# Kernel tuning notes

Measured on AMD Instinct MI355X. Metric: run time of the kernel, lower is better.

## Reference

```python
import jax, jax.numpy as jnp
import numpy as np

EPS = 1e-8


def setup_inputs() -> dict:
    key = jax.random.key(0)
    k1, k2 = jax.random.split(key)
    B, C, L = 16, 4, 4096
    K, S = 256, 128
    x = jax.random.normal(k1, (B, C, L), dtype=jnp.float32)
    shapelets = jax.random.normal(k2, (C, K, S), dtype=jnp.float32)
    return {"x": x, "shapelets": shapelets}


def reference(x, shapelets):
    # x: (B, C, L); shapelets: (C, K, S)
    B, C, L = x.shape
    _, K, S = shapelets.shape
    W = L - S + 1  # number of sliding windows

    # unfold: (B, C, W, S) sliding windows with stride 1
    idx = jnp.arange(W)[:, None] + jnp.arange(S)[None, :]  # (W, S)
    win = x[:, :, idx]  # (B, C, W, S)
    win = win / jnp.maximum(jnp.linalg.norm(win, axis=-1, keepdims=True), EPS)

    shp = shapelets / jnp.maximum(
        jnp.linalg.norm(shapelets, axis=-1, keepdims=True), EPS
    )  # (C, K, S)

    # pairwise dot products: (B, C, W, K)
    sim = jnp.einsum("bcws,cks->bcwk", win, shp)
    # sum over channels, keepdim, transpose(2,3), divide by n_dims
    sim = jnp.sum(sim, axis=1, keepdims=True) / C  # (B, 1, W, K)
    sim = jnp.transpose(sim, (0, 1, 3, 2))  # (B, 1, K, W)
    sim = jax.nn.relu(sim)
    # global max-pool over window positions -> (B, 1, K)
    return jnp.max(sim, axis=3)
```

## Files before the change

kernel.cpp:

```cpp
#include <hip/hip_runtime.h>
#include <hip/hip_bf16.h>

#define NB 16
#define NC 4
#define NL 4096
#define NK 256
#define NS 128
#define NW (NL - NS + 1)
#define WPB 512
#define KPB 128
#define XEL 640
#define XROW 656
#define EPSF 1e-8f

typedef __attribute__((ext_vector_type(8))) _Float16 f16x8;
typedef __attribute__((ext_vector_type(2))) _Float16 f16x2;
typedef __attribute__((ext_vector_type(4))) float floatx4;

typedef __attribute__((address_space(3))) unsigned int* lds_ptr_t;
typedef const __attribute__((address_space(1))) unsigned int* gbl_ptr_t;

__device__ inline short f2h(float f) {
    _Float16 h = (_Float16)f;
    short s;
    __builtin_memcpy(&s, &h, sizeof(short));
    return s;
}

__device__ inline void gload_lds16(const void* g, void* l) {
    __builtin_amdgcn_global_load_lds((gbl_ptr_t)g, (lds_ptr_t)l, 16, 0, 0);
}

__global__ __launch_bounds__(64)
void norm_shp_kernel(const float* __restrict__ shp, short* __restrict__ shpn) {
    int ck = blockIdx.x;
    int k = ck & (NK - 1);
    int lane = threadIdx.x;
    const float* p = shp + (size_t)ck * NS;
    float v0 = p[lane];
    float v1 = p[lane + 64];
    float ss = v0 * v0 + v1 * v1;
    #pragma unroll
    for (int o = 32; o > 0; o >>= 1) ss += __shfl_xor(ss, o, 64);
    float rn = 1.f / fmaxf(sqrtf(ss), EPSF);
    int s0 = lane, s1 = lane + 64;
    int d0 = ((((s0 >> 3) ^ (k & 15)) << 3) | (s0 & 7));
    int d1 = ((((s1 >> 3) ^ (k & 15)) << 3) | (s1 & 7));
    shpn[(size_t)ck * NS + d0] = f2h(v0 * rn);
    shpn[(size_t)ck * NS + d1] = f2h(v1 * rn);
}

__global__ __launch_bounds__(512, 1)
void mcs_main_kernel(const float* __restrict__ x,
                     const short* __restrict__ shpn,
                     float* __restrict__ out) {
    __shared__ f16x8 bs[NC][KPB * 16];
    __shared__ alignas(16) short xcp[NC][4][XROW];
    __shared__ union {
        float scratch[NC][XEL];
        struct { float invw[NC][WPB]; float epi[8][64]; } c;
    } u;

    const int kq = blockIdx.x, slot = blockIdx.y;
    const int b = slot >> 3, wslot = slot & 7;
    const int w0 = wslot * WPB;
    const int tid = threadIdx.x;
    const int lane = tid & 63, wv = tid >> 6;
    const int m = lane & 15, q = lane >> 4, r = m & 3;
    const int kh = wv & 1, wh = wv >> 1;

    {
        const char* gbase = (const char*)shpn + (size_t)(kq * KPB) * NS * 2;
        #pragma unroll
        for (int c = 0; c < NC; c++) {
            const char* gc = gbase + (size_t)c * NK * NS * 2;
            char* lc = (char*)&bs[c][0];
            #pragma unroll
            for (int i = 0; i < 4; i++) {
                int off = (wv * 4 + i) * 1024;
                gload_lds16(gc + off + lane * 16, lc + off);
            }
        }
    }

    float xv[NC], xv2[NC];
    {
        const int g0 = w0 + tid;
        #pragma unroll
        for (int c = 0; c < NC; c++)
            xv[c] = (g0 < NL) ? x[((size_t)b * NC + c) * NL + g0] : 0.f;
        if (tid < XEL - 512) {
            const int g1 = g0 + 512;
            #pragma unroll
            for (int c = 0; c < NC; c++)
                xv2[c] = (g1 < NL) ? x[((size_t)b * NC + c) * NL + g1] : 0.f;
        }
    }

    #pragma unroll
    for (int c = 0; c < NC; c++) {
        short hv = f2h(xv[c]);
        #pragma unroll
        for (int rr = 0; rr < 4; rr++) {
            int o2 = tid - rr;
            if (o2 >= 0) xcp[c][rr][o2] = hv;
        }
        u.scratch[c][tid] = xv[c] * xv[c];
        if (tid < XEL - 512) {
            short hv2 = f2h(xv2[c]);
            #pragma unroll
            for (int rr = 0; rr < 4; rr++)
                xcp[c][rr][tid + 512 - rr] = hv2;
            u.scratch[c][tid + 512] = xv2[c] * xv2[c];
        }
    }
    __syncthreads();

    if (wv < 4) {
        const int c = wv;
        const int base = lane * 10;
        float v[10];
        #pragma unroll
        for (int i = 0; i < 10; i++) v[i] = u.scratch[c][base + i];
        #pragma unroll
        for (int i = 1; i < 10; i++) v[i] += v[i - 1];
        float tt = v[9];
        #pragma unroll
        for (int o = 1; o < 64; o <<= 1) {
            float uu = __shfl_up(tt, o, 64);
            if (lane >= o) tt += uu;
        }
        float excl = tt - v[9];
        #pragma unroll
        for (int i = 0; i < 10; i++) u.scratch[c][base + i] = v[i] + excl;
    }
    __syncthreads();

    float ivreg[4];
    #pragma unroll
    for (int i = 0; i < 4; i++) {
        int ii = tid + 512 * i;
        int c = ii >> 9, o = ii & 511;
        float nn = u.scratch[c][o + 127] - (o ? u.scratch[c][o - 1] : 0.f);
        int w = w0 + o;
        ivreg[i] = (w < NW) ? 1.f / fmaxf(sqrtf(fmaxf(nn, 0.f)), EPSF) : 0.f;
    }
    __syncthreads();
    #pragma unroll
    for (int i = 0; i < 4; i++) {
        int ii = tid + 512 * i;
        u.c.invw[ii >> 9][ii & 511] = ivreg[i];
    }
    asm volatile("s_waitcnt vmcnt(0)" ::: "memory");
    __syncthreads();

    floatx4 tot[8][4];
    #pragma unroll
    for (int mt = 0; mt < 8; mt++)
        #pragma unroll
        for (int kt = 0; kt < 4; kt++)
            tot[mt][kt] = (floatx4){0.f, 0.f, 0.f, 0.f};

    #pragma unroll
    for (int c = 0; c < NC; c++) {
        f16x2 iv2[8];
        #pragma unroll
        for (int mt = 0; mt < 8; mt++) {
            _Float16 ih = (_Float16)u.c.invw[c][wh * 128 + mt * 16 + m];
            iv2[mt] = (f16x2){ih, ih};
        }
        #pragma unroll
        for (int s0 = 0; s0 < NS; s0 += 32) {
            f16x8 a[8];
            #pragma unroll
            for (int mt = 0; mt < 8; mt++) {
                int ts = wh * 128 + mt * 16 + m + s0 + q * 8;
                const uint2* pp = (const uint2*)&xcp[c][r][ts - r];
                union { uint2 uu[2]; f16x8 v; f16x2 h2[4]; } cv;
                cv.uu[0] = pp[0]; cv.uu[1] = pp[1];
                #pragma unroll
                for (int p2 = 0; p2 < 4; p2++) cv.h2[p2] *= iv2[mt];
                a[mt] = cv.v;
            }
            int cc = (s0 >> 3) + q;
            #pragma unroll
            for (int kt = 0; kt < 4; kt++) {
                int k = kh * 64 + kt * 16 + m;
                f16x8 bf = bs[c][(k << 4) | (cc ^ m)];
                #pragma unroll
                for (int mt = 0; mt < 8; mt++)
                    tot[mt][kt] = __builtin_amdgcn_mfma_f32_16x16x32_f16(
                        a[mt], bf, tot[mt][kt], 0, 0, 0);
            }
        }
    }

    #pragma unroll
    for (int kt = 0; kt < 4; kt++) {
        float mx = -1e30f;
        #pragma unroll
        for (int mt = 0; mt < 8; mt++) {
            floatx4 v = tot[mt][kt];
            mx = fmaxf(mx, fmaxf(fmaxf(v.x, v.y), fmaxf(v.z, v.w)));
        }
        mx = fmaxf(mx, __shfl_xor(mx, 16, 64));
        mx = fmaxf(mx, __shfl_xor(mx, 32, 64));
        if (lane < 16) u.c.epi[wv][kt * 16 + lane] = mx;
    }
    __syncthreads();
    if (tid < 128) {
        int kh_ = tid >> 6, j = tid & 63;
        float v = fmaxf(fmaxf(u.c.epi[kh_][j],     u.c.epi[kh_ + 2][j]),
                        fmaxf(u.c.epi[kh_ + 4][j], u.c.epi[kh_ + 6][j]));
        v = fmaxf(v, 0.f) * 0.25f;
        atomicMax((int*)out + (size_t)b * NK + kq * KPB + tid,
                  __float_as_int(v));
    }
}

extern "C" void kernel_launch(void* const* d_in, const int* in_sizes, int n_in,
                              void* d_out, int out_size, void* d_ws, size_t ws_size,
                              hipStream_t stream) {
    (void)in_sizes; (void)n_in; (void)out_size; (void)ws_size;
    const float* x   = (const float*)d_in[0];
    const float* shp = (const float*)d_in[1];
    float* out = (float*)d_out;

    short* shpn = (short*)d_ws;

    norm_shp_kernel<<<NC * NK, 64, 0, stream>>>(shp, shpn);
    mcs_main_kernel<<<dim3(2, 128), 512, 0, stream>>>(x, shpn, out);
}
```

Baseline: 70.25 us.

## Software-pipeline LDS fragment loads with MFMA using ping-pong register buffers

Restructures the channel/s0 MFMA loop into a flattened 16-iteration software pipeline that splits the A tiles into two halves and double-buffers both A and B fragments in registers, so the LDS reads for the next step are issued while the current MFMAs run. It also raises wave priority around the MFMA bursts with s_setprio. The cost it targets is LDS latency stalls between fragment loads and the matrix ops. In exchange the code is more complex and needs more registers, which could cause spills at 512 threads per block.

```diff
diff --git a/kernel.cpp b/kernel.cpp
--- a/kernel.cpp
+++ b/kernel.cpp
@@ -161,37 +161,78 @@
         for (int kt = 0; kt < 4; kt++)
             tot[mt][kt] = (floatx4){0.f, 0.f, 0.f, 0.f};
 
-    #pragma unroll
-    for (int c = 0; c < NC; c++) {
-        f16x2 iv2[8];
+    f16x8 aA[4], aB[4], bA[4], bB[4];
+    f16x2 iv[8];
+
+    auto loadIv = [&](int c) {
         #pragma unroll
         for (int mt = 0; mt < 8; mt++) {
             _Float16 ih = (_Float16)u.c.invw[c][wh * 128 + mt * 16 + m];
-            iv2[mt] = (f16x2){ih, ih};
-        }
-        #pragma unroll
-        for (int s0 = 0; s0 < NS; s0 += 32) {
-            f16x8 a[8];
-            #pragma unroll
-            for (int mt = 0; mt < 8; mt++) {
-                int ts = wh * 128 + mt * 16 + m + s0 + q * 8;
-                const uint2* pp = (const uint2*)&xcp[c][r][ts - r];
-                union { uint2 uu[2]; f16x8 v; f16x2 h2[4]; } cv;
-                cv.uu[0] = pp[0]; cv.uu[1] = pp[1];
-                #pragma unroll
-                for (int p2 = 0; p2 < 4; p2++) cv.h2[p2] *= iv2[mt];
-                a[mt] = cv.v;
-            }
-            int cc = (s0 >> 3) + q;
-            #pragma unroll
-            for (int kt = 0; kt < 4; kt++) {
-                int k = kh * 64 + kt * 16 + m;
-                f16x8 bf = bs[c][(k << 4) | (cc ^ m)];
-                #pragma unroll
-                for (int mt = 0; mt < 8; mt++)
-                    tot[mt][kt] = __builtin_amdgcn_mfma_f32_16x16x32_f16(
-                        a[mt], bf, tot[mt][kt], 0, 0, 0);
-            }
+            iv[mt] = (f16x2){ih, ih};
+        }
+    };
+    auto loadA4 = [&](int c, int s0, int g, f16x8* a) {
+        #pragma unroll
+        for (int i = 0; i < 4; i++) {
+            int mt = g * 4 + i;
+            int ts = wh * 128 + mt * 16 + m + s0 + q * 8;
+            const uint2* pp = (const uint2*)&xcp[c][r][ts - r];
+            union { uint2 uu[2]; f16x8 v; } cv;
+            cv.uu[0] = pp[0]; cv.uu[1] = pp[1];
+            a[i] = cv.v;
+        }
+    };
+    auto loadB4 = [&](int c, int s0, f16x8* bv) {
+        int cc = (s0 >> 3) + q;
+        #pragma unroll
+        for (int kt = 0; kt < 4; kt++) {
+            int k = kh * 64 + kt * 16 + m;
+            bv[kt] = bs[c][(k << 4) | (cc ^ m)];
+        }
+    };
+    auto mm16 = [&](int g, f16x8* a, f16x8* bv) {
+        #pragma unroll
+        for (int i = 0; i < 4; i++) {
+            union { f16x8 v; f16x2 h2[4]; } cv;
+            cv.v = a[i];
+            #pragma unroll
+            for (int p2 = 0; p2 < 4; p2++) cv.h2[p2] *= iv[g * 4 + i];
+            a[i] = cv.v;
+        }
+        __builtin_amdgcn_s_setprio(1);
+        #pragma unroll
+        for (int kt = 0; kt < 4; kt++)
+            #pragma unroll
+            for (int i = 0; i < 4; i++)
+                tot[g * 4 + i][kt] = __builtin_amdgcn_mfma_f32_16x16x32_f16(
+                    a[i], bv[kt], tot[g * 4 + i][kt], 0, 0, 0);
+        __builtin_amdgcn_s_setprio(0);
+    };
+
+    loadIv(0);
+    loadA4(0, 0, 0, aA);
+    loadB4(0, 0, bA);
+    #pragma unroll
+    for (int ip = 0; ip < 8; ip++) {
+        {
+            const int it = 2 * ip, c = it >> 2, s0 = (it & 3) * 32;
+            const int cn = (it + 1) >> 2, sn = ((it + 1) & 3) * 32;
+            loadA4(c, s0, 1, aB);
+            mm16(0, aA, bA);
+            loadA4(cn, sn, 0, aA);
+            loadB4(cn, sn, bB);
+            mm16(1, aB, bA);
+        }
+        {
+            const int it = 2 * ip + 1, c = it >> 2, s0 = (it & 3) * 32;
+            const bool last = (it == 15);
+            const int cn = last ? c : (it + 1) >> 2;
+            const int sn = last ? s0 : ((it + 1) & 3) * 32;
+            loadA4(c, s0, 1, aB);
+            mm16(0, aA, bB);
+            if (!last) { loadA4(cn, sn, 0, aA); loadB4(cn, sn, bA); }
+            mm16(1, aB, bB);
+            if ((it & 3) == 3 && !last) loadIv(cn);
         }
     }
 
```

Result: slower. 71.97 us (+2.4%).

## Reuse overlapping window fragments across m-tiles and preload all B fragments

Applied to the files above, without the earlier changes.

Restructures the MFMA inner loop to exploit Toeplitz structure: the A fragment for (mt, s0) equals the one for (mt+2, s0-32), so each LDS-loaded x fragment is reused across diagonals rather than reloaded per (mt, s0). All 16 B fragments per channel are hoisted into registers up front, and the next A fragment is software-prefetched while s_setprio raises priority around the MFMA bursts. This cuts LDS reads for A but raises register pressure from holding 16 B fragments.

```diff
diff --git a/kernel.cpp b/kernel.cpp
--- a/kernel.cpp
+++ b/kernel.cpp
@@ -163,35 +163,47 @@
 
     #pragma unroll
     for (int c = 0; c < NC; c++) {
-        f16x2 iv2[8];
+        f16x2 iv[8];
         #pragma unroll
         for (int mt = 0; mt < 8; mt++) {
             _Float16 ih = (_Float16)u.c.invw[c][wh * 128 + mt * 16 + m];
-            iv2[mt] = (f16x2){ih, ih};
-        }
-        #pragma unroll
-        for (int s0 = 0; s0 < NS; s0 += 32) {
-            f16x8 a[8];
-            #pragma unroll
-            for (int mt = 0; mt < 8; mt++) {
-                int ts = wh * 128 + mt * 16 + m + s0 + q * 8;
-                const uint2* pp = (const uint2*)&xcp[c][r][ts - r];
-                union { uint2 uu[2]; f16x8 v; f16x2 h2[4]; } cv;
-                cv.uu[0] = pp[0]; cv.uu[1] = pp[1];
-                #pragma unroll
-                for (int p2 = 0; p2 < 4; p2++) cv.h2[p2] *= iv2[mt];
-                a[mt] = cv.v;
-            }
-            int cc = (s0 >> 3) + q;
+            iv[mt] = (f16x2){ih, ih};
+        }
+        f16x8 bh[16];
+        #pragma unroll
+        for (int si = 0; si < 4; si++) {
+            int cc = si * 4 + q;
             #pragma unroll
             for (int kt = 0; kt < 4; kt++) {
                 int k = kh * 64 + kt * 16 + m;
-                f16x8 bf = bs[c][(k << 4) | (cc ^ m)];
-                #pragma unroll
-                for (int mt = 0; mt < 8; mt++)
-                    tot[mt][kt] = __builtin_amdgcn_mfma_f32_16x16x32_f16(
-                        a[mt], bf, tot[mt][kt], 0, 0, 0);
-            }
+                bh[si * 4 + kt] = bs[c][(k << 4) | (cc ^ m)];
+            }
+        }
+        const uint2* ap =
+            (const uint2*)&xcp[c][r][wh * 128 + m + q * 8 - r];
+        union { uint2 uu[2]; f16x8 v; f16x2 h2[4]; } aC, aN, sc;
+        aC.uu[0] = ap[0]; aC.uu[1] = ap[1];
+        #pragma unroll
+        for (int d = 0; d < 14; d++) {
+            if (d < 13) {
+                aN.uu[0] = ap[d * 4 + 4]; aN.uu[1] = ap[d * 4 + 5];
+            }
+            __builtin_amdgcn_s_setprio(1);
+            #pragma unroll
+            for (int j = 0; j < 4; j++) {
+                const int mt = d - 2 * j;
+                if (mt >= 0 && mt < 8) {
+                    sc.v = aC.v;
+                    #pragma unroll
+                    for (int p2 = 0; p2 < 4; p2++) sc.h2[p2] *= iv[mt];
+                    #pragma unroll
+                    for (int kt = 0; kt < 4; kt++)
+                        tot[mt][kt] = __builtin_amdgcn_mfma_f32_16x16x32_f16(
+                            sc.v, bh[j * 4 + kt], tot[mt][kt], 0, 0, 0);
+                }
+            }
+            __builtin_amdgcn_s_setprio(0);
+            aC.v = aN.v;
         }
     }
 
```

Result: slower. 72.11 us (+2.7%).
